# Performance work log

Measured on AMD Instinct MI355X. Metric: run time of the kernel, lower is better.

The kernel has to match this reference:

```python
import jax, jax.numpy as jnp
import numpy as np

B, T, D = 8, 1024, 1024
H, HS = 16, 64  # num_heads, head_size; H*HS == D


def setup_inputs() -> dict:
    key = jax.random.key(0)
    ks = jax.random.split(key, 5)
    scale = 0.02
    x = jax.random.normal(ks[0], (B, T, D), dtype=jnp.float32)
    Wq = jax.random.normal(ks[1], (H, D, HS), dtype=jnp.float32) * scale
    Wk = jax.random.normal(ks[2], (H, D, HS), dtype=jnp.float32) * scale
    Wv = jax.random.normal(ks[3], (H, D, HS), dtype=jnp.float32) * scale
    Wo = jax.random.normal(ks[4], (D, D), dtype=jnp.float32) * scale
    bo = jnp.zeros((D,), dtype=jnp.float32)
    return {"x": x, "Wq": Wq, "Wk": Wk, "Wv": Wv, "Wo": Wo, "bo": bo}


def reference(x, Wq, Wk, Wv, Wo, bo):
    # Per-head linear projections (bias-free, as in Head): [B,H,T,HS]
    q = jnp.einsum('btd,hds->bhts', x, Wq)
    k = jnp.einsum('btd,hds->bhts', x, Wk)
    v = jnp.einsum('btd,hds->bhts', x, Wv)
    # Scaled scores with causal mask: [B,H,T,T]
    scores = jnp.einsum('bhts,bhus->bhtu', q, k) * (HS ** -0.5)
    causal = jnp.tril(jnp.ones((T, T), dtype=bool))
    scores = jnp.where(causal, scores, jnp.finfo(scores.dtype).min)
    att = jax.nn.softmax(scores, axis=-1)
    # Weighted sum over values, then concat heads: [B,T,H*HS]
    out = jnp.einsum('bhtu,bhus->bhts', att, v)
    out = out.transpose(0, 2, 1, 3).reshape(B, T, H * HS)
    # Output projection (nn.Linear: y = x @ W^T + b)
    return out @ Wo.T + bo
```

## Files before the change

### kernel.cpp

```cpp
#include <hip/hip_runtime.h>
#include <hip/hip_bf16.h>

#define BBATCH 8
#define TSEQ   1024
#define DMODEL 1024
#define NHEAD  16
#define HSZ    64

typedef unsigned short ushort_t;
typedef __attribute__((ext_vector_type(8))) short short8;
typedef __attribute__((ext_vector_type(4))) float float4v;

__device__ __forceinline__ ushort_t f2bf(float f) {
    __hip_bfloat16 h = __float2bfloat16(f);
    return *reinterpret_cast<ushort_t*>(&h);
}
__device__ __forceinline__ ushort_t f2bf_fast(float f) {
    return (ushort_t)((__float_as_uint(f) + 0x8000u) >> 16);
}
__device__ __forceinline__ unsigned int pack_bf2(float lo, float hi) {
    unsigned int a = __float_as_uint(lo) + 0x8000u;
    unsigned int b = __float_as_uint(hi) + 0x8000u;
    return __builtin_amdgcn_perm(b, a, 0x07060302u);
}

__device__ __forceinline__ short8 cvt8(const float* f) {
    union { ushort_t u[8]; short8 v; } r;
    #pragma unroll
    for (int e = 0; e < 8; ++e) r.u[e] = f2bf(f[e]);
    return r.v;
}

__device__ __forceinline__ void async16(const ushort_t* g, ushort_t* l) {
    __builtin_amdgcn_global_load_lds(
        (const __attribute__((address_space(1))) unsigned int*)g,
        (__attribute__((address_space(3))) unsigned int*)l, 16, 0, 0);
}

template<int N> __device__ __forceinline__ void vwait() {
    if constexpr (N == 3)      asm volatile("s_waitcnt vmcnt(3)" ::: "memory");
    else if constexpr (N == 0) asm volatile("s_waitcnt vmcnt(0)" ::: "memory");
}

__global__ __launch_bounds__(256) void cvt_f32_bf16(
    const float* __restrict__ src, ushort_t* __restrict__ dst)
{
    const size_t idx = ((size_t)blockIdx.x * 256 + threadIdx.x) * 16;
    float f[16];
    *(float4*)(f + 0)  = *(const float4*)(src + idx);
    *(float4*)(f + 4)  = *(const float4*)(src + idx + 4);
    *(float4*)(f + 8)  = *(const float4*)(src + idx + 8);
    *(float4*)(f + 12) = *(const float4*)(src + idx + 12);
    uint4 o0 = make_uint4(pack_bf2(f[0], f[1]),   pack_bf2(f[2], f[3]),
                          pack_bf2(f[4], f[5]),   pack_bf2(f[6], f[7]));
    uint4 o1 = make_uint4(pack_bf2(f[8], f[9]),   pack_bf2(f[10], f[11]),
                          pack_bf2(f[12], f[13]), pack_bf2(f[14], f[15]));
    *(uint4*)(dst + idx) = o0;
    *(uint4*)(dst + idx + 8) = o1;
}

__global__ __launch_bounds__(256) void pack_w(
    const float* __restrict__ Wq, const float* __restrict__ Wk,
    const float* __restrict__ Wv, ushort_t* __restrict__ WpT)
{
    __shared__ ushort_t L[64 * 72];
    const int tid = threadIdx.x;
    const int d0 = blockIdx.x * 64;
    const int wh = blockIdx.y;
    const int w = wh >> 4, h = wh & 15;
    const float* W = (w == 0 ? Wq : (w == 1 ? Wk : Wv)) + (size_t)h * DMODEL * HSZ;

    int dr = tid >> 2, sc = (tid & 3) * 16;
    const float4* src = (const float4*)(W + (size_t)(d0 + dr) * HSZ + sc);
    float f[16];
    *(float4*)(f + 0) = src[0]; *(float4*)(f + 4) = src[1];
    *(float4*)(f + 8) = src[2]; *(float4*)(f + 12) = src[3];
    *(short8*)(L + dr * 72 + sc)     = cvt8(f);
    *(short8*)(L + dr * 72 + sc + 8) = cvt8(f + 8);
    __syncthreads();

    int s = tid >> 2, dc = (tid & 3) * 16;
    union { ushort_t u[16]; short8 v[2]; } o;
    #pragma unroll
    for (int j = 0; j < 16; ++j) o.u[j] = L[(dc + j) * 72 + s];
    ushort_t* dst = WpT + (size_t)(w * 1024 + h * 64 + s) * DMODEL + d0 + dc;
    *(short8*)dst = o.v[0];
    *(short8*)(dst + 8) = o.v[1];
}

template<bool STG, int VW>
__device__ __forceinline__ void kstep32(
    const ushort_t* Ab, const ushort_t* Bb,
    ushort_t* An, ushort_t* Bn,
    const ushort_t*& gA, const ushort_t*& gB,
    const int wave,
    const int (&aoff)[4], const int (&boff)[4],
    float4v (&acc)[4][4])
{
    short8 av[4], bv[4];
    #pragma unroll
    for (int a = 0; a < 4; ++a) av[a] = *(const short8*)(Ab + aoff[a]);
    #pragma unroll
    for (int b = 0; b < 4; ++b) bv[b] = *(const short8*)(Bb + boff[b]);
    if (STG) {
        async16(gA,                An + wave * 512);
        async16(gB,                Bn + wave * 512);
        async16(gB + 128 * DMODEL, Bn + 4096 + wave * 512);
        gA += 32; gB += 32;
    }
    __builtin_amdgcn_s_setprio(1);
    #pragma unroll
    for (int a = 0; a < 4; ++a)
        #pragma unroll
        for (int b = 0; b < 4; ++b)
            acc[a][b] = __builtin_amdgcn_mfma_f32_16x16x32_bf16(
                av[a], bv[b], acc[a][b], 0, 0, 0);
    __builtin_amdgcn_s_setprio(0);
    vwait<VW>();
    __builtin_amdgcn_s_barrier();
}

__global__ __launch_bounds__(512, 4) void qkv_gemm(
    const ushort_t* __restrict__ Xb, const ushort_t* __restrict__ WpT,
    ushort_t* __restrict__ Qb, ushort_t* __restrict__ Kb, ushort_t* __restrict__ Vt)
{
    __shared__ ushort_t Ab[3][128 * 32];
    __shared__ ushort_t Bb[3][256 * 32];

    const int tid = threadIdx.x;
    const int wave = tid >> 6, lane = tid & 63;
    const int q = lane >> 4, cc = lane & 15;
    const int wm = wave >> 2, wn = wave & 3;

    const int bid = blockIdx.x;
    const int xcd = bid & 7;
    const bool isV = (bid >= 512);
    int ta, tb;
    if (!isV) {
        int lo = bid >> 3;
        ta = lo >> 2;
        tb = xcd * 4 + (lo & 3);
    } else {
        int lo = (bid - 512) >> 3;
        ta = xcd * 8 + (lo & 7);
        tb = lo >> 3;
    }
    const ushort_t* pA = isV ? Xb  + (size_t)ta * 128 * DMODEL
                             : WpT + (size_t)ta * 128 * DMODEL;
    const ushort_t* pB = isV ? WpT + (size_t)(2048 + tb * 256) * DMODEL
                             : Xb  + (size_t)tb * 256 * DMODEL;

    const int srow = lane >> 2;
    const int chx = (lane & 3) ^ ((lane >> 3) & 3);
    const ushort_t* gA = pA + (size_t)(wave * 16 + srow) * DMODEL + chx * 8;
    const ushort_t* gB = pB + (size_t)(wave * 16 + srow) * DMODEL + chx * 8;

    int aoff[4], boff[4];
    const int cswz = (q ^ ((cc >> 1) & 3)) * 8;
    #pragma unroll
    for (int f = 0; f < 4; ++f) {
        aoff[f] = (wm * 64 + f * 16 + cc) * 32 + cswz;
        boff[f] = (wn * 64 + f * 16 + cc) * 32 + cswz;
    }

    float4v acc[4][4];
    #pragma unroll
    for (int a = 0; a < 4; ++a)
        #pragma unroll
        for (int b = 0; b < 4; ++b) acc[a][b] = (float4v){0.f, 0.f, 0.f, 0.f};

    async16(gA,                Ab[0] + wave * 512);
    async16(gB,                Bb[0] + wave * 512);
    async16(gB + 128 * DMODEL, Bb[0] + 4096 + wave * 512);
    gA += 32; gB += 32;
    async16(gA,                Ab[1] + wave * 512);
    async16(gB,                Bb[1] + wave * 512);
    async16(gB + 128 * DMODEL, Bb[1] + 4096 + wave * 512);
    gA += 32; gB += 32;
    vwait<3>();
    __builtin_amdgcn_s_barrier();

    #pragma unroll 1
    for (int it = 0; it < 10; ++it) {
        kstep32<true, 3>(Ab[0], Bb[0], Ab[2], Bb[2], gA, gB, wave, aoff, boff, acc);
        kstep32<true, 3>(Ab[1], Bb[1], Ab[0], Bb[0], gA, gB, wave, aoff, boff, acc);
        kstep32<true, 3>(Ab[2], Bb[2], Ab[1], Bb[1], gA, gB, wave, aoff, boff, acc);
    }
    kstep32<false, 0>(Ab[0], Bb[0], Ab[2], Bb[2], gA, gB, wave, aoff, boff, acc);
    kstep32<false, -1>(Ab[1], Bb[1], Ab[0], Bb[0], gA, gB, wave, aoff, boff, acc);

    if (!isV) {
        ushort_t* Out = (ta < 8) ? Qb : Kb;
        const float osc = (ta < 8) ? 0.18033688011112042f : 1.0f;
        const int h = ((ta * 128 + wm * 64) >> 6) & 15;
        #pragma unroll
        for (int b = 0; b < 4; ++b) {
            int mc = tb * 256 + wn * 64 + b * 16 + cc;
            int bb = mc >> 10, t = mc & 1023;
            size_t rb = (((size_t)(bb * NHEAD + h)) * TSEQ + t) * HSZ;
            #pragma unroll
            for (int a = 0; a < 4; ++a) {
                int s0 = a * 16 + q * 4;
                uint2 pk = make_uint2(
                    pack_bf2(acc[a][b][0] * osc, acc[a][b][1] * osc),
                    pack_bf2(acc[a][b][2] * osc, acc[a][b][3] * osc));
                *(uint2*)(Out + rb + s0) = pk;
            }
        }
    } else {
        #pragma unroll
        for (int b = 0; b < 4; ++b) {
            int nc = tb * 256 + wn * 64 + b * 16 + cc;
            int h = nc >> 6, s = nc & 63;
            #pragma unroll
            for (int a = 0; a < 4; ++a) {
                int mr = ta * 128 + wm * 64 + a * 16 + q * 4;
                int bb = mr >> 10, t0 = mr & 1023;
                size_t addr = (((size_t)(bb * NHEAD + h)) * HSZ + s) * TSEQ + t0;
                uint2 pk = make_uint2(pack_bf2(acc[a][b][0], acc[a][b][1]),
                                      pack_bf2(acc[a][b][2], acc[a][b][3]));
                *(uint2*)(Vt + addr) = pk;
            }
        }
    }
}

__global__ __launch_bounds__(256) void attn(
    const ushort_t* __restrict__ Qb, const ushort_t* __restrict__ Kb,
    const ushort_t* __restrict__ Vt, ushort_t* __restrict__ Ob)
{
    __shared__ ushort_t Ks[2][64 * 64];
    __shared__ ushort_t VTs[2][64 * 64];
    __shared__ ushort_t Ps[4][32 * 72];
    const int tid = threadIdx.x;
    const int wave = tid >> 6, lane = tid & 63;
    const int q = lane >> 4, cc = lane & 15;
    const int bid = blockIdx.x;
    const int qt = 7 - (bid >> 7);
    const int bh = bid & 127;
    const size_t base = (size_t)bh * TSEQ * HSZ;
    const int J = 2 * qt + 2;

    const ushort_t* kg[2]; const ushort_t* vg[2]; int dmo[2];
    #pragma unroll
    for (int i = 0; i < 2; ++i) {
        int rr = wave * 16 + i * 8 + (lane >> 3);
        int ch = (lane & 7) ^ (rr & 7);
        kg[i] = Kb + base + (size_t)rr * HSZ + ch * 8;
        vg[i] = Vt + base + (size_t)rr * TSEQ + ch * 8;
        dmo[i] = (wave * 16 + i * 8) * 64;
    }

    short8 qf[2][2];
    #pragma unroll
    for (int tt = 0; tt < 2; ++tt) {
        const ushort_t* qp = Qb + base +
            (size_t)(qt * 128 + wave * 32 + tt * 16 + cc) * HSZ + q * 8;
        qf[tt][0] = *(const short8*)qp;
        qf[tt][1] = *(const short8*)(qp + 32);
    }

    int koff[4][2], poff[2][2];
    #pragma unroll
    for (int ut = 0; ut < 4; ++ut)
        #pragma unroll
        for (int kt = 0; kt < 2; ++kt)
            koff[ut][kt] = (ut * 16 + cc) * 64 + (((kt * 4 + q) ^ (cc & 7)) * 8);
    #pragma unroll
    for (int tt = 0; tt < 2; ++tt)
        #pragma unroll
        for (int kt = 0; kt < 2; ++kt)
            poff[tt][kt] = (tt * 16 + cc) * 72 + kt * 32 + q * 8;

    float4v oacc[2][4];
    #pragma unroll
    for (int tt = 0; tt < 2; ++tt)
        #pragma unroll
        for (int st = 0; st < 4; ++st) oacc[tt][st] = (float4v){0.f, 0.f, 0.f, 0.f};
    float lsum[2] = {0.f, 0.f};

    #pragma unroll
    for (int i = 0; i < 2; ++i) {
        async16(kg[i], &Ks[0][dmo[i]]);
        async16(vg[i], &VTs[0][dmo[i]]);
    }
    __syncthreads();

    for (int jt = 0; jt < J; ++jt) {
        const ushort_t* Kc = Ks[jt & 1];
        const ushort_t* Vc = VTs[jt & 1];
        if (jt + 1 < J) {
            int nb = (jt + 1) & 1;
            #pragma unroll
            for (int i = 0; i < 2; ++i) {
                async16(kg[i] + (size_t)(jt + 1) * 64 * HSZ, &Ks[nb][dmo[i]]);
                async16(vg[i] + (jt + 1) * 64, &VTs[nb][dmo[i]]);
            }
        }

        float4v sc[4][2];
        #pragma unroll
        for (int ut = 0; ut < 4; ++ut)
            #pragma unroll
            for (int tt = 0; tt < 2; ++tt) sc[ut][tt] = (float4v){0.f, 0.f, 0.f, 0.f};
        #pragma unroll
        for (int kt = 0; kt < 2; ++kt) {
            short8 kf[4];
            #pragma unroll
            for (int ut = 0; ut < 4; ++ut) kf[ut] = *(const short8*)(Kc + koff[ut][kt]);
            #pragma unroll
            for (int ut = 0; ut < 4; ++ut) {
                sc[ut][0] = __builtin_amdgcn_mfma_f32_16x16x32_bf16(
                    kf[ut], qf[0][kt], sc[ut][0], 0, 0, 0);
                sc[ut][1] = __builtin_amdgcn_mfma_f32_16x16x32_bf16(
                    kf[ut], qf[1][kt], sc[ut][1], 0, 0, 0);
            }
        }

        if ((jt >> 1) == qt) {
            #pragma unroll
            for (int tt = 0; tt < 2; ++tt) {
                const int tg = qt * 128 + wave * 32 + tt * 16 + cc;
                #pragma unroll
                for (int ut = 0; ut < 4; ++ut) {
                    float pv[4]; float ps = 0.f;
                    #pragma unroll
                    for (int rr = 0; rr < 4; ++rr) {
                        float p = exp2f(sc[ut][tt][rr]);
                        if ((jt * 64 + ut * 16 + q * 4 + rr) > tg) p = 0.f;
                        pv[rr] = p; ps += p;
                    }
                    lsum[tt] += ps;
                    *(uint2*)&Ps[wave][(tt * 16 + cc) * 72 + ut * 16 + q * 4] =
                        make_uint2(pack_bf2(pv[0], pv[1]), pack_bf2(pv[2], pv[3]));
                }
            }
        } else {
            #pragma unroll
            for (int tt = 0; tt < 2; ++tt) {
                #pragma unroll
                for (int ut = 0; ut < 4; ++ut) {
                    float pv[4]; float ps = 0.f;
                    #pragma unroll
                    for (int rr = 0; rr < 4; ++rr) {
                        float p = exp2f(sc[ut][tt][rr]);
                        pv[rr] = p; ps += p;
                    }
                    lsum[tt] += ps;
                    *(uint2*)&Ps[wave][(tt * 16 + cc) * 72 + ut * 16 + q * 4] =
                        make_uint2(pack_bf2(pv[0], pv[1]), pack_bf2(pv[2], pv[3]));
                }
            }
        }

        #pragma unroll
        for (int kt = 0; kt < 2; ++kt) {
            short8 pa0 = *(const short8*)&Ps[wave][poff[0][kt]];
            short8 pa1 = *(const short8*)&Ps[wave][poff[1][kt]];
            #pragma unroll
            for (int st = 0; st < 4; ++st) {
                short8 vf = *(const short8*)(Vc + koff[st][kt]);
                oacc[0][st] = __builtin_amdgcn_mfma_f32_16x16x32_bf16(
                    pa0, vf, oacc[0][st], 0, 0, 0);
                oacc[1][st] = __builtin_amdgcn_mfma_f32_16x16x32_bf16(
                    pa1, vf, oacc[1][st], 0, 0, 0);
            }
        }
        __syncthreads();
    }

    float inv[2];
    #pragma unroll
    for (int tt = 0; tt < 2; ++tt) {
        float l = lsum[tt];
        l += __shfl_xor(l, 16);
        l += __shfl_xor(l, 32);
        inv[tt] = 1.f / l;
    }
    const int b = bh >> 4, h = bh & 15;
    #pragma unroll
    for (int tt = 0; tt < 2; ++tt)
        #pragma unroll
        for (int rr = 0; rr < 4; ++rr) {
            float iv = __shfl(inv[tt], q * 4 + rr);
            int t = qt * 128 + wave * 32 + tt * 16 + q * 4 + rr;
            size_t rb = ((size_t)b * TSEQ + t) * DMODEL + h * HSZ;
            #pragma unroll
            for (int st = 0; st < 4; ++st)
                Ob[rb + st * 16 + cc] = f2bf_fast(oacc[tt][st][rr] * iv);
        }
}

__global__ __launch_bounds__(256) void oproj_gemm(
    const ushort_t* __restrict__ Obuf, const ushort_t* __restrict__ Wob,
    const float* __restrict__ bo, float* __restrict__ out)
{
    __shared__ ushort_t As[128 * 64];
    __shared__ ushort_t Bs[128 * 64];
    const int tid = threadIdx.x;
    const int wave = tid >> 6, lane = tid & 63;
    const int q = lane >> 4, cc = lane & 15;
    const int bid = blockIdx.x;
    const int xcd = bid & 7, local = bid >> 3;
    const int n0 = (local >> 3) * 128;
    const int m0 = (xcd * 8 + (local & 7)) * 128;
    const int wm = wave >> 1, wn = wave & 1;

    const ushort_t* ag[4]; const ushort_t* bg[4]; int lo_[4];
    #pragma unroll
    for (int i = 0; i < 4; ++i) {
        int row = wave * 32 + i * 8 + (lane >> 3);
        int ch = (lane & 7) ^ (row & 7);
        ag[i] = Obuf + (size_t)(m0 + row) * DMODEL + ch * 8;
        bg[i] = Wob + (size_t)(n0 + row) * DMODEL + ch * 8;
        lo_[i] = (wave * 32 + i * 8) * 64;
    }
    int aoff[4][2], boff[4][2];
    #pragma unroll
    for (int mt = 0; mt < 4; ++mt) {
        int row = wm * 64 + mt * 16 + cc;
        #pragma unroll
        for (int kt = 0; kt < 2; ++kt)
            aoff[mt][kt] = row * 64 + (((kt * 4 + q) ^ (row & 7)) * 8);
    }
    #pragma unroll
    for (int nt = 0; nt < 4; ++nt) {
        int row = wn * 64 + nt * 16 + cc;
        #pragma unroll
        for (int kt = 0; kt < 2; ++kt)
            boff[nt][kt] = row * 64 + (((kt * 4 + q) ^ (row & 7)) * 8);
    }

    float4v acc[4][4];
    #pragma unroll
    for (int a = 0; a < 4; ++a)
        #pragma unroll
        for (int b = 0; b < 4; ++b) acc[a][b] = (float4v){0.f, 0.f, 0.f, 0.f};

    for (int j = 0; j < 16; ++j) {
        #pragma unroll
        for (int i = 0; i < 4; ++i) {
            async16(ag[i], As + lo_[i]);
            async16(bg[i], Bs + lo_[i]);
            ag[i] += 64; bg[i] += 64;
        }
        __syncthreads();

        short8 av[4][2], bv[4][2];
        #pragma unroll
        for (int mt = 0; mt < 4; ++mt) {
            av[mt][0] = *(const short8*)(As + aoff[mt][0]);
            av[mt][1] = *(const short8*)(As + aoff[mt][1]);
        }
        #pragma unroll
        for (int nt = 0; nt < 4; ++nt) {
            bv[nt][0] = *(const short8*)(Bs + boff[nt][0]);
            bv[nt][1] = *(const short8*)(Bs + boff[nt][1]);
        }
        #pragma unroll
        for (int kt = 0; kt < 2; ++kt)
            #pragma unroll
            for (int mt = 0; mt < 4; ++mt)
                #pragma unroll
                for (int nt = 0; nt < 4; ++nt)
                    acc[mt][nt] = __builtin_amdgcn_mfma_f32_16x16x32_bf16(
                        av[mt][kt], bv[nt][kt], acc[mt][nt], 0, 0, 0);
        __syncthreads();
    }

    #pragma unroll
    for (int nt = 0; nt < 4; ++nt) {
        int n = n0 + wn * 64 + nt * 16 + cc;
        float bias = bo[n];
        #pragma unroll
        for (int mt = 0; mt < 4; ++mt)
            #pragma unroll
            for (int rr = 0; rr < 4; ++rr) {
                int m = m0 + wm * 64 + mt * 16 + q * 4 + rr;
                out[(size_t)m * DMODEL + n] = acc[mt][nt][rr] + bias;
            }
    }
}

extern "C" void kernel_launch(void* const* d_in, const int* in_sizes, int n_in,
                              void* d_out, int out_size, void* d_ws, size_t ws_size,
                              hipStream_t stream)
{
    const float* x  = (const float*)d_in[0];
    const float* Wq = (const float*)d_in[1];
    const float* Wk = (const float*)d_in[2];
    const float* Wv = (const float*)d_in[3];
    const float* Wo = (const float*)d_in[4];
    const float* bo = (const float*)d_in[5];
    float* out = (float*)d_out;

    const size_t SEG = (size_t)8 * 1024 * 1024;
    ushort_t* Qb  = (ushort_t*)d_ws;
    ushort_t* Kb  = Qb + SEG;
    ushort_t* Vtb = Kb + SEG;
    ushort_t* WpT = Vtb + SEG;
    ushort_t* Ob  = WpT;
    ushort_t* Xb  = (ushort_t*)d_out;
    ushort_t* Wob = Qb;

    cvt_f32_bf16<<<dim3(2048),    256, 0, stream>>>(x, Xb);
    pack_w      <<<dim3(16, 48),  256, 0, stream>>>(Wq, Wk, Wv, WpT);
    qkv_gemm    <<<dim3(768),     512, 0, stream>>>(Xb, WpT, Qb, Kb, Vtb);
    attn        <<<dim3(1024),    256, 0, stream>>>(Qb, Kb, Vtb, Ob);
    cvt_f32_bf16<<<dim3(256),     256, 0, stream>>>(Wo, Wob);
    oproj_gemm  <<<dim3(512),     256, 0, stream>>>(Ob, Wob, bo, out);
}
```

Measured before the change: 226.1 us.

## Enlarge attention query tile to 256 rows with 8 waves and per-wave causal skip

The attention kernel now uses 512-thread blocks covering 256 query rows (8 waves of 32 rows), halving the grid. Each K/V tile staged in shared memory is reused by twice as many query rows, and each thread loads one chunk instead of two. Waves whose rows lie entirely before the current key tile skip compute with a per-wave causal bound, but still take part in the barriers. This cuts K/V global traffic at the cost of fewer blocks, coarser causal load balance and more shared memory per block. The GEMM loop is also pulled out into helper functions with no change in behaviour.

New measurement: 229.8 us. About the same (+1.7%).

```diff
diff --git a/kernel.cpp b/kernel.cpp
--- a/kernel.cpp
+++ b/kernel.cpp
@@ -120,6 +120,31 @@
     __builtin_amdgcn_s_barrier();
 }
 
+__device__ __forceinline__ void gemm_loop32(
+    ushort_t (*Ab)[128 * 32], ushort_t (*Bb)[256 * 32],
+    const ushort_t*& gA, const ushort_t*& gB, const int wave,
+    const int (&aoff)[4], const int (&boff)[4], float4v (&acc)[4][4])
+{
+    #pragma unroll 1
+    for (int it = 0; it < 10; ++it) {
+        kstep32<true, 3>(Ab[0], Bb[0], Ab[2], Bb[2], gA, gB, wave, aoff, boff, acc);
+        kstep32<true, 3>(Ab[1], Bb[1], Ab[0], Bb[0], gA, gB, wave, aoff, boff, acc);
+        kstep32<true, 3>(Ab[2], Bb[2], Ab[1], Bb[1], gA, gB, wave, aoff, boff, acc);
+    }
+    kstep32<false, 0>(Ab[0], Bb[0], Ab[2], Bb[2], gA, gB, wave, aoff, boff, acc);
+    kstep32<false, -1>(Ab[1], Bb[1], Ab[0], Bb[0], gA, gB, wave, aoff, boff, acc);
+}
+
+__device__ __forceinline__ void stage_full(
+    ushort_t* Abuf, ushort_t* Bbuf,
+    const ushort_t*& gA, const ushort_t*& gB, const int wave)
+{
+    async16(gA,                Abuf + wave * 512);
+    async16(gB,                Bbuf + wave * 512);
+    async16(gB + 128 * DMODEL, Bbuf + 4096 + wave * 512);
+    gA += 32; gB += 32;
+}
+
 __global__ __launch_bounds__(512, 4) void qkv_gemm(
     const ushort_t* __restrict__ Xb, const ushort_t* __restrict__ WpT,
     ushort_t* __restrict__ Qb, ushort_t* __restrict__ Kb, ushort_t* __restrict__ Vt)
@@ -169,25 +194,12 @@
         #pragma unroll
         for (int b = 0; b < 4; ++b) acc[a][b] = (float4v){0.f, 0.f, 0.f, 0.f};
 
-    async16(gA,                Ab[0] + wave * 512);
-    async16(gB,                Bb[0] + wave * 512);
-    async16(gB + 128 * DMODEL, Bb[0] + 4096 + wave * 512);
-    gA += 32; gB += 32;
-    async16(gA,                Ab[1] + wave * 512);
-    async16(gB,                Bb[1] + wave * 512);
-    async16(gB + 128 * DMODEL, Bb[1] + 4096 + wave * 512);
-    gA += 32; gB += 32;
+    stage_full(Ab[0], Bb[0], gA, gB, wave);
+    stage_full(Ab[1], Bb[1], gA, gB, wave);
     vwait<3>();
     __builtin_amdgcn_s_barrier();
 
-    #pragma unroll 1
-    for (int it = 0; it < 10; ++it) {
-        kstep32<true, 3>(Ab[0], Bb[0], Ab[2], Bb[2], gA, gB, wave, aoff, boff, acc);
-        kstep32<true, 3>(Ab[1], Bb[1], Ab[0], Bb[0], gA, gB, wave, aoff, boff, acc);
-        kstep32<true, 3>(Ab[2], Bb[2], Ab[1], Bb[1], gA, gB, wave, aoff, boff, acc);
-    }
-    kstep32<false, 0>(Ab[0], Bb[0], Ab[2], Bb[2], gA, gB, wave, aoff, boff, acc);
-    kstep32<false, -1>(Ab[1], Bb[1], Ab[0], Bb[0], gA, gB, wave, aoff, boff, acc);
+    gemm_loop32(Ab, Bb, gA, gB, wave, aoff, boff, acc);
 
     if (!isV) {
         ushort_t* Out = (ta < 8) ? Qb : Kb;
@@ -225,37 +237,35 @@
     }
 }
 
-__global__ __launch_bounds__(256) void attn(
+__global__ __launch_bounds__(512, 4) void attn(
     const ushort_t* __restrict__ Qb, const ushort_t* __restrict__ Kb,
     const ushort_t* __restrict__ Vt, ushort_t* __restrict__ Ob)
 {
     __shared__ ushort_t Ks[2][64 * 64];
     __shared__ ushort_t VTs[2][64 * 64];
-    __shared__ ushort_t Ps[4][32 * 72];
+    __shared__ ushort_t Ps[8][32 * 72];
     const int tid = threadIdx.x;
     const int wave = tid >> 6, lane = tid & 63;
     const int q = lane >> 4, cc = lane & 15;
     const int bid = blockIdx.x;
-    const int qt = 7 - (bid >> 7);
+    const int qt = 3 - (bid >> 7);
     const int bh = bid & 127;
     const size_t base = (size_t)bh * TSEQ * HSZ;
-    const int J = 2 * qt + 2;
-
-    const ushort_t* kg[2]; const ushort_t* vg[2]; int dmo[2];
-    #pragma unroll
-    for (int i = 0; i < 2; ++i) {
-        int rr = wave * 16 + i * 8 + (lane >> 3);
-        int ch = (lane & 7) ^ (rr & 7);
-        kg[i] = Kb + base + (size_t)rr * HSZ + ch * 8;
-        vg[i] = Vt + base + (size_t)rr * TSEQ + ch * 8;
-        dmo[i] = (wave * 16 + i * 8) * 64;
-    }
+    const int J = 4 * qt + 4;
+    const int wbase = qt * 256 + wave * 32;
+    const int wmax = (wbase + 31) >> 6;
+
+    const int rr = wave * 8 + (lane >> 3);
+    const int ch = (lane & 7) ^ (rr & 7);
+    const ushort_t* kg = Kb + base + (size_t)rr * HSZ + ch * 8;
+    const ushort_t* vg = Vt + base + (size_t)rr * TSEQ + ch * 8;
+    const int dmo = wave * 512;
 
     short8 qf[2][2];
     #pragma unroll
     for (int tt = 0; tt < 2; ++tt) {
         const ushort_t* qp = Qb + base +
-            (size_t)(qt * 128 + wave * 32 + tt * 16 + cc) * HSZ + q * 8;
+            (size_t)(wbase + tt * 16 + cc) * HSZ + q * 8;
         qf[tt][0] = *(const short8*)qp;
         qf[tt][1] = *(const short8*)(qp + 32);
     }
@@ -279,11 +289,8 @@
         for (int st = 0; st < 4; ++st) oacc[tt][st] = (float4v){0.f, 0.f, 0.f, 0.f};
     float lsum[2] = {0.f, 0.f};
 
-    #pragma unroll
-    for (int i = 0; i < 2; ++i) {
-        async16(kg[i], &Ks[0][dmo[i]]);
-        async16(vg[i], &VTs[0][dmo[i]]);
-    }
+    async16(kg, &Ks[0][dmo]);
+    async16(vg, &VTs[0][dmo]);
     __syncthreads();
 
     for (int jt = 0; jt < J; ++jt) {
@@ -291,79 +298,78 @@
         const ushort_t* Vc = VTs[jt & 1];
         if (jt + 1 < J) {
             int nb = (jt + 1) & 1;
-            #pragma unroll
-            for (int i = 0; i < 2; ++i) {
-                async16(kg[i] + (size_t)(jt + 1) * 64 * HSZ, &Ks[nb][dmo[i]]);
-                async16(vg[i] + (jt + 1) * 64, &VTs[nb][dmo[i]]);
-            }
-        }
-
-        float4v sc[4][2];
-        #pragma unroll
-        for (int ut = 0; ut < 4; ++ut)
-            #pragma unroll
-            for (int tt = 0; tt < 2; ++tt) sc[ut][tt] = (float4v){0.f, 0.f, 0.f, 0.f};
-        #pragma unroll
-        for (int kt = 0; kt < 2; ++kt) {
-            short8 kf[4];
-            #pragma unroll
-            for (int ut = 0; ut < 4; ++ut) kf[ut] = *(const short8*)(Kc + koff[ut][kt]);
-            #pragma unroll
-            for (int ut = 0; ut < 4; ++ut) {
-                sc[ut][0] = __builtin_amdgcn_mfma_f32_16x16x32_bf16(
-                    kf[ut], qf[0][kt], sc[ut][0], 0, 0, 0);
-                sc[ut][1] = __builtin_amdgcn_mfma_f32_16x16x32_bf16(
-                    kf[ut], qf[1][kt], sc[ut][1], 0, 0, 0);
-            }
-        }
-
-        if ((jt >> 1) == qt) {
-            #pragma unroll
-            for (int tt = 0; tt < 2; ++tt) {
-                const int tg = qt * 128 + wave * 32 + tt * 16 + cc;
+            async16(kg + (size_t)(jt + 1) * 64 * HSZ, &Ks[nb][dmo]);
+            async16(vg + (jt + 1) * 64, &VTs[nb][dmo]);
+        }
+
+        if (jt <= wmax) {
+            float4v sc[4][2];
+            #pragma unroll
+            for (int ut = 0; ut < 4; ++ut)
+                #pragma unroll
+                for (int tt = 0; tt < 2; ++tt) sc[ut][tt] = (float4v){0.f, 0.f, 0.f, 0.f};
+            #pragma unroll
+            for (int kt = 0; kt < 2; ++kt) {
+                short8 kf[4];
+                #pragma unroll
+                for (int ut = 0; ut < 4; ++ut) kf[ut] = *(const short8*)(Kc + koff[ut][kt]);
                 #pragma unroll
                 for (int ut = 0; ut < 4; ++ut) {
-                    float pv[4]; float ps = 0.f;
-                    #pragma unroll
-                    for (int rr = 0; rr < 4; ++rr) {
-                        float p = exp2f(sc[ut][tt][rr]);
-                        if ((jt * 64 + ut * 16 + q * 4 + rr) > tg) p = 0.f;
-                        pv[rr] = p; ps += p;
-                    }
-                    lsum[tt] += ps;
-                    *(uint2*)&Ps[wave][(tt * 16 + cc) * 72 + ut * 16 + q * 4] =
-                        make_uint2(pack_bf2(pv[0], pv[1]), pack_bf2(pv[2], pv[3]));
+                    sc[ut][0] = __builtin_amdgcn_mfma_f32_16x16x32_bf16(
+                        kf[ut], qf[0][kt], sc[ut][0], 0, 0, 0);
+                    sc[ut][1] = __builtin_amdgcn_mfma_f32_16x16x32_bf16(
+                        kf[ut], qf[1][kt], sc[ut][1], 0, 0, 0);
                 }
             }
-        } else {
-            #pragma unroll
-            for (int tt = 0; tt < 2; ++tt) {
-                #pragma unroll
-                for (int ut = 0; ut < 4; ++ut) {
-                    float pv[4]; float ps = 0.f;
+
+            if (jt == wmax) {
+                #pragma unroll
+                for (int tt = 0; tt < 2; ++tt) {
+                    const int tg = wbase + tt * 16 + cc;
                     #pragma unroll
-                    for (int rr = 0; rr < 4; ++rr) {
-                        float p = exp2f(sc[ut][tt][rr]);
-                        pv[rr] = p; ps += p;
+                    for (int ut = 0; ut < 4; ++ut) {
+                        float pv[4]; float ps = 0.f;
+                        #pragma unroll
+                        for (int rr2 = 0; rr2 < 4; ++rr2) {
+                            float p = exp2f(sc[ut][tt][rr2]);
+                            if ((jt * 64 + ut * 16 + q * 4 + rr2) > tg) p = 0.f;
+                            pv[rr2] = p; ps += p;
+                        }
+                        lsum[tt] += ps;
+                        *(uint2*)&Ps[wave][(tt * 16 + cc) * 72 + ut * 16 + q * 4] =
+                            make_uint2(pack_bf2(pv[0], pv[1]), pack_bf2(pv[2], pv[3]));
                     }
-                    lsum[tt] += ps;
-                    *(uint2*)&Ps[wave][(tt * 16 + cc) * 72 + ut * 16 + q * 4] =
-                        make_uint2(pack_bf2(pv[0], pv[1]), pack_bf2(pv[2], pv[3]));
+                }
+            } else {
+                #pragma unroll
+                for (int tt = 0; tt < 2; ++tt) {
+                    #pragma unroll
+                    for (int ut = 0; ut < 4; ++ut) {
+                        float pv[4]; float ps = 0.f;
+                        #pragma unroll
+                        for (int rr2 = 0; rr2 < 4; ++rr2) {
+                            float p = exp2f(sc[ut][tt][rr2]);
+                            pv[rr2] = p; ps += p;
+                        }
+                        lsum[tt] += ps;
+                        *(uint2*)&Ps[wave][(tt * 16 + cc) * 72 + ut * 16 + q * 4] =
+                            make_uint2(pack_bf2(pv[0], pv[1]), pack_bf2(pv[2], pv[3]));
+                    }
                 }
             }
-        }
-
-        #pragma unroll
-        for (int kt = 0; kt < 2; ++kt) {
-            short8 pa0 = *(const short8*)&Ps[wave][poff[0][kt]];
-            short8 pa1 = *(const short8*)&Ps[wave][poff[1][kt]];
-            #pragma unroll
-            for (int st = 0; st < 4; ++st) {
-                short8 vf = *(const short8*)(Vc + koff[st][kt]);
-                oacc[0][st] = __builtin_amdgcn_mfma_f32_16x16x32_bf16(
-                    pa0, vf, oacc[0][st], 0, 0, 0);
-                oacc[1][st] = __builtin_amdgcn_mfma_f32_16x16x32_bf16(
-                    pa1, vf, oacc[1][st], 0, 0, 0);
+
+            #pragma unroll
+            for (int kt = 0; kt < 2; ++kt) {
+                short8 pa0 = *(const short8*)&Ps[wave][poff[0][kt]];
+                short8 pa1 = *(const short8*)&Ps[wave][poff[1][kt]];
+                #pragma unroll
+                for (int st = 0; st < 4; ++st) {
+                    short8 vf = *(const short8*)(Vc + koff[st][kt]);
+                    oacc[0][st] = __builtin_amdgcn_mfma_f32_16x16x32_bf16(
+                        pa0, vf, oacc[0][st], 0, 0, 0);
+                    oacc[1][st] = __builtin_amdgcn_mfma_f32_16x16x32_bf16(
+                        pa1, vf, oacc[1][st], 0, 0, 0);
+                }
             }
         }
         __syncthreads();
@@ -381,13 +387,13 @@
     #pragma unroll
     for (int tt = 0; tt < 2; ++tt)
         #pragma unroll
-        for (int rr = 0; rr < 4; ++rr) {
-            float iv = __shfl(inv[tt], q * 4 + rr);
-            int t = qt * 128 + wave * 32 + tt * 16 + q * 4 + rr;
+        for (int rr2 = 0; rr2 < 4; ++rr2) {
+            float iv = __shfl(inv[tt], q * 4 + rr2);
+            int t = wbase + tt * 16 + q * 4 + rr2;
             size_t rb = ((size_t)b * TSEQ + t) * DMODEL + h * HSZ;
             #pragma unroll
             for (int st = 0; st < 4; ++st)
-                Ob[rb + st * 16 + cc] = f2bf_fast(oacc[tt][st][rr] * iv);
+                Ob[rb + st * 16 + cc] = f2bf_fast(oacc[tt][st][rr2] * iv);
         }
 }
 
@@ -506,7 +512,7 @@
     cvt_f32_bf16<<<dim3(2048),    256, 0, stream>>>(x, Xb);
     pack_w      <<<dim3(16, 48),  256, 0, stream>>>(Wq, Wk, Wv, WpT);
     qkv_gemm    <<<dim3(768),     512, 0, stream>>>(Xb, WpT, Qb, Kb, Vtb);
-    attn        <<<dim3(1024),    256, 0, stream>>>(Qb, Kb, Vtb, Ob);
+    attn        <<<dim3(512),     512, 0, stream>>>(Qb, Kb, Vtb, Ob);
     cvt_f32_bf16<<<dim3(256),     256, 0, stream>>>(Wo, Wob);
     oproj_gemm  <<<dim3(512),     256, 0, stream>>>(Ob, Wob, bo, out);
 }
```

## Load K/V fragments directly from global memory in attention, dropping LDS staging

Applied to the files above, without the earlier changes.

The attention kernel no longer stages K and V^T tiles through double-buffered shared memory with async copies and block barriers. Each wave now reads its MFMA operand fragments straight from global memory, relying on L1/L2 to serve the four waves that share a tile. This removes the LDS footprint and the per-iteration __syncthreads, but makes all four waves fetch the same K/V data with no prefetch ahead of use, so global load latency is exposed. The GEMM part only moves code into helper functions.

Measured after the change: 258.8 us. 14.5% more time.

```diff
diff --git a/kernel.cpp b/kernel.cpp
--- a/kernel.cpp
+++ b/kernel.cpp
@@ -120,6 +120,31 @@
     __builtin_amdgcn_s_barrier();
 }
 
+__device__ __forceinline__ void gemm_loop32(
+    ushort_t (*Ab)[128 * 32], ushort_t (*Bb)[256 * 32],
+    const ushort_t*& gA, const ushort_t*& gB, const int wave,
+    const int (&aoff)[4], const int (&boff)[4], float4v (&acc)[4][4])
+{
+    #pragma unroll 1
+    for (int it = 0; it < 10; ++it) {
+        kstep32<true, 3>(Ab[0], Bb[0], Ab[2], Bb[2], gA, gB, wave, aoff, boff, acc);
+        kstep32<true, 3>(Ab[1], Bb[1], Ab[0], Bb[0], gA, gB, wave, aoff, boff, acc);
+        kstep32<true, 3>(Ab[2], Bb[2], Ab[1], Bb[1], gA, gB, wave, aoff, boff, acc);
+    }
+    kstep32<false, 0>(Ab[0], Bb[0], Ab[2], Bb[2], gA, gB, wave, aoff, boff, acc);
+    kstep32<false, -1>(Ab[1], Bb[1], Ab[0], Bb[0], gA, gB, wave, aoff, boff, acc);
+}
+
+__device__ __forceinline__ void stage_full(
+    ushort_t* Abuf, ushort_t* Bbuf,
+    const ushort_t*& gA, const ushort_t*& gB, const int wave)
+{
+    async16(gA,                Abuf + wave * 512);
+    async16(gB,                Bbuf + wave * 512);
+    async16(gB + 128 * DMODEL, Bbuf + 4096 + wave * 512);
+    gA += 32; gB += 32;
+}
+
 __global__ __launch_bounds__(512, 4) void qkv_gemm(
     const ushort_t* __restrict__ Xb, const ushort_t* __restrict__ WpT,
     ushort_t* __restrict__ Qb, ushort_t* __restrict__ Kb, ushort_t* __restrict__ Vt)
@@ -169,25 +194,12 @@
         #pragma unroll
         for (int b = 0; b < 4; ++b) acc[a][b] = (float4v){0.f, 0.f, 0.f, 0.f};
 
-    async16(gA,                Ab[0] + wave * 512);
-    async16(gB,                Bb[0] + wave * 512);
-    async16(gB + 128 * DMODEL, Bb[0] + 4096 + wave * 512);
-    gA += 32; gB += 32;
-    async16(gA,                Ab[1] + wave * 512);
-    async16(gB,                Bb[1] + wave * 512);
-    async16(gB + 128 * DMODEL, Bb[1] + 4096 + wave * 512);
-    gA += 32; gB += 32;
+    stage_full(Ab[0], Bb[0], gA, gB, wave);
+    stage_full(Ab[1], Bb[1], gA, gB, wave);
     vwait<3>();
     __builtin_amdgcn_s_barrier();
 
-    #pragma unroll 1
-    for (int it = 0; it < 10; ++it) {
-        kstep32<true, 3>(Ab[0], Bb[0], Ab[2], Bb[2], gA, gB, wave, aoff, boff, acc);
-        kstep32<true, 3>(Ab[1], Bb[1], Ab[0], Bb[0], gA, gB, wave, aoff, boff, acc);
-        kstep32<true, 3>(Ab[2], Bb[2], Ab[1], Bb[1], gA, gB, wave, aoff, boff, acc);
-    }
-    kstep32<false, 0>(Ab[0], Bb[0], Ab[2], Bb[2], gA, gB, wave, aoff, boff, acc);
-    kstep32<false, -1>(Ab[1], Bb[1], Ab[0], Bb[0], gA, gB, wave, aoff, boff, acc);
+    gemm_loop32(Ab, Bb, gA, gB, wave, aoff, boff, acc);
 
     if (!isV) {
         ushort_t* Out = (ta < 8) ? Qb : Kb;
@@ -229,8 +241,6 @@
     const ushort_t* __restrict__ Qb, const ushort_t* __restrict__ Kb,
     const ushort_t* __restrict__ Vt, ushort_t* __restrict__ Ob)
 {
-    __shared__ ushort_t Ks[2][64 * 64];
-    __shared__ ushort_t VTs[2][64 * 64];
     __shared__ ushort_t Ps[4][32 * 72];
     const int tid = threadIdx.x;
     const int wave = tid >> 6, lane = tid & 63;
@@ -241,16 +251,6 @@
     const size_t base = (size_t)bh * TSEQ * HSZ;
     const int J = 2 * qt + 2;
 
-    const ushort_t* kg[2]; const ushort_t* vg[2]; int dmo[2];
-    #pragma unroll
-    for (int i = 0; i < 2; ++i) {
-        int rr = wave * 16 + i * 8 + (lane >> 3);
-        int ch = (lane & 7) ^ (rr & 7);
-        kg[i] = Kb + base + (size_t)rr * HSZ + ch * 8;
-        vg[i] = Vt + base + (size_t)rr * TSEQ + ch * 8;
-        dmo[i] = (wave * 16 + i * 8) * 64;
-    }
-
     short8 qf[2][2];
     #pragma unroll
     for (int tt = 0; tt < 2; ++tt) {
@@ -260,12 +260,10 @@
         qf[tt][1] = *(const short8*)(qp + 32);
     }
 
-    int koff[4][2], poff[2][2];
-    #pragma unroll
-    for (int ut = 0; ut < 4; ++ut)
-        #pragma unroll
-        for (int kt = 0; kt < 2; ++kt)
-            koff[ut][kt] = (ut * 16 + cc) * 64 + (((kt * 4 + q) ^ (cc & 7)) * 8);
+    const ushort_t* kp = Kb + base + (size_t)cc * HSZ + q * 8;
+    const ushort_t* vp = Vt + base + (size_t)cc * TSEQ + q * 8;
+
+    int poff[2][2];
     #pragma unroll
     for (int tt = 0; tt < 2; ++tt)
         #pragma unroll
@@ -279,25 +277,7 @@
         for (int st = 0; st < 4; ++st) oacc[tt][st] = (float4v){0.f, 0.f, 0.f, 0.f};
     float lsum[2] = {0.f, 0.f};
 
-    #pragma unroll
-    for (int i = 0; i < 2; ++i) {
-        async16(kg[i], &Ks[0][dmo[i]]);
-        async16(vg[i], &VTs[0][dmo[i]]);
-    }
-    __syncthreads();
-
     for (int jt = 0; jt < J; ++jt) {
-        const ushort_t* Kc = Ks[jt & 1];
-        const ushort_t* Vc = VTs[jt & 1];
-        if (jt + 1 < J) {
-            int nb = (jt + 1) & 1;
-            #pragma unroll
-            for (int i = 0; i < 2; ++i) {
-                async16(kg[i] + (size_t)(jt + 1) * 64 * HSZ, &Ks[nb][dmo[i]]);
-                async16(vg[i] + (jt + 1) * 64, &VTs[nb][dmo[i]]);
-            }
-        }
-
         float4v sc[4][2];
         #pragma unroll
         for (int ut = 0; ut < 4; ++ut)
@@ -307,7 +287,9 @@
         for (int kt = 0; kt < 2; ++kt) {
             short8 kf[4];
             #pragma unroll
-            for (int ut = 0; ut < 4; ++ut) kf[ut] = *(const short8*)(Kc + koff[ut][kt]);
+            for (int ut = 0; ut < 4; ++ut)
+                kf[ut] = *(const short8*)(kp +
+                    (size_t)(jt * 64 + ut * 16) * HSZ + kt * 32);
             #pragma unroll
             for (int ut = 0; ut < 4; ++ut) {
                 sc[ut][0] = __builtin_amdgcn_mfma_f32_16x16x32_bf16(
@@ -359,14 +341,14 @@
             short8 pa1 = *(const short8*)&Ps[wave][poff[1][kt]];
             #pragma unroll
             for (int st = 0; st < 4; ++st) {
-                short8 vf = *(const short8*)(Vc + koff[st][kt]);
+                short8 vf = *(const short8*)(vp +
+                    (size_t)(st * 16) * TSEQ + jt * 64 + kt * 32);
                 oacc[0][st] = __builtin_amdgcn_mfma_f32_16x16x32_bf16(
                     pa0, vf, oacc[0][st], 0, 0, 0);
                 oacc[1][st] = __builtin_amdgcn_mfma_f32_16x16x32_bf16(
                     pa1, vf, oacc[1][st], 0, 0, 0);
             }
         }
-        __syncthreads();
     }
 
     float inv[2];
```
